# Kernel tuning notes

Measured on AMD Instinct MI355X. Metric: run time of the kernel, lower is better.

Reference implementation:

```python
import jax, jax.numpy as jnp
import numpy as np

DETER, STOCH, ACT, HID, RANK, B = 2048, 1024, 12, 1024, 16, 16384
EPS = 1e-4


def rmsnorm(x, w, eps=EPS):
    # RMSNorm with learnable scale (torch nn.RMSNorm default affine)
    return x * jax.lax.rsqrt(jnp.mean(x * x, axis=-1, keepdims=True) + eps) * w


def setup_inputs() -> dict:
    key = jax.random.key(0)
    ks = jax.random.split(key, 16)
    s = 0.02
    return {
        "stoch": jax.random.normal(ks[0], (B, 32, 32), jnp.float32),
        "deter": jax.random.normal(ks[1], (B, DETER), jnp.float32),
        "action": jax.random.normal(ks[2], (B, ACT), jnp.float32),
        "W1": jax.random.normal(ks[3], (STOCH + ACT, HID), jnp.float32) * s,
        "b1": jnp.zeros((HID,), jnp.float32),
        "g1": jnp.ones((HID,), jnp.float32),
        "W2": jax.random.normal(ks[4], (HID, DETER), jnp.float32) * s,
        "b2": jnp.zeros((DETER,), jnp.float32),
        "Wu": jax.random.normal(ks[5], (DETER, RANK), jnp.float32) * s,
        "Wv": jax.random.normal(ks[6], (RANK, DETER), jnp.float32) * s,
        "a_log": jnp.zeros((DETER,), jnp.float32),
        "dt_p": jnp.zeros((DETER,), jnp.float32),
        "Wg": jax.random.normal(ks[7], (2 * DETER, DETER), jnp.float32) * s,
        "bg": jnp.zeros((DETER,), jnp.float32),
        "Wc": jax.random.normal(ks[8], (2 * DETER, DETER), jnp.float32) * s,
        "bc": jnp.zeros((DETER,), jnp.float32),
        "gn": jnp.ones((DETER,), jnp.float32),
    }


def reference(stoch, deter, action, W1, b1, g1, W2, b2, Wu, Wv, a_log, dt_p,
              Wg, bg, Wc, bc, gn):
    bsz = action.shape[0]
    s = stoch.reshape(bsz, -1)
    # action / clip(|action|, min=1) with detached denominator
    denom = jax.lax.stop_gradient(jnp.maximum(jnp.abs(action), 1.0))
    a_n = action / denom
    # input MLP: Linear -> RMSNorm -> SiLU -> Linear
    x = jnp.concatenate([s, a_n], axis=-1) @ W1 + b1
    x = jax.nn.silu(rmsnorm(x, g1))
    inp = x @ W2 + b2                                # [B, deter]
    # low-rank state mixing
    mixed = deter + (deter @ Wu) @ Wv                # [B, deter]
    dt = jax.nn.softplus(dt_p)[None, :] + 1e-4       # [1, deter]
    a = -jax.nn.softplus(a_log)[None, :]
    ssm = jnp.exp(a * dt) * mixed + dt * inp
    joint = jnp.concatenate([ssm, inp], axis=-1)     # [B, 2*deter]
    gate = jax.nn.sigmoid(joint @ Wg + bg)
    cand = jnp.tanh(joint @ Wc + bc)
    out = gate * cand + (1.0 - gate) * deter
    return rmsnorm(out, gn)
```

## Files before the change

kernel.cpp:

```cpp
#include <hip/hip_runtime.h>
#include <hip/hip_bf16.h>
#include <stdint.h>

#define DETER 2048
#define STOCH 1024
#define ACT   12
#define HID   1024
#define RANK  16
#define BSZ   16384
#define K1P   1056

typedef unsigned short u16;
typedef __attribute__((ext_vector_type(8))) short short8;
typedef __attribute__((ext_vector_type(4))) float f32x4;

__device__ __forceinline__ float bf2f(u16 u) {
  union { uint32_t i; float f; } c; c.i = ((uint32_t)u) << 16; return c.f;
}
__device__ __forceinline__ u16 f2bf(float f) {
  union { float f; uint32_t u; } c; c.f = f;
  uint32_t r = ((c.u >> 16) & 1u) + 0x7fffu;
  return (u16)((c.u + r) >> 16);
}
__device__ __forceinline__ float sigmoidf_(float x) { return 1.f / (1.f + expf(-x)); }
__device__ __forceinline__ float softplusf_(float x) { return (x > 20.f) ? x : log1pf(expf(x)); }

__device__ __forceinline__ void gload_lds16(const void* g, void* l) {
  __builtin_amdgcn_global_load_lds((const __attribute__((address_space(1))) void*)g,
                                   (__attribute__((address_space(3))) void*)l, 16, 0, 0);
}

#define SZ_WBT1 ((size_t)1024 * K1P * 2)
#define SZ_WBT2 ((size_t)DETER * HID * 2)
#define SZ_WBTG ((size_t)DETER * (2 * DETER) * 2)
#define SZ_XIN  ((size_t)BSZ * K1P * 2)
#define SZ_H    ((size_t)BSZ * HID * 2)
#define SZ_XPRE ((size_t)BSZ * HID * 4)
#define SZ_J    ((size_t)BSZ * (2 * DETER) * 2)

#define O_WBT1 ((size_t)0)
#define O_WBT2 (O_WBT1 + SZ_WBT1)
#define O_WBTG (O_WBT2 + SZ_WBT2)
#define O_WBTC (O_WBTG + SZ_WBTG)
#define O_E    (O_WBTC + SZ_WBTG)
#define O_DTV  (O_E + 8192)
#define O_XIN  (O_DTV + 8192)
#define O_H    (O_XIN + SZ_XIN)
#define O_XPRE (O_H + SZ_H)
#define O_J    (O_XPRE + SZ_XPRE)
#define O_CPRE O_XIN
#define O_SSMA O_XPRE
#define O_GPRE O_XPRE
#define WS_NEED (O_J + SZ_J)

__global__ void prep_params(const float* __restrict__ a_log, const float* __restrict__ dt_p,
                            float* __restrict__ ev, float* __restrict__ dtv) {
  int j = blockIdx.x * 256 + threadIdx.x;
  if (j < DETER) {
    float dt = softplusf_(dt_p[j]) + 1e-4f;
    float a  = -softplusf_(a_log[j]);
    ev[j]  = expf(a * dt);
    dtv[j] = dt;
  }
}

__global__ void transpose_w(const float* __restrict__ in, u16* __restrict__ out,
                            int K, int N, int Kp) {
  __shared__ float tile[32][33];
  int k0 = blockIdx.x * 32, n0 = blockIdx.y * 32;
  int tx = threadIdx.x, ty = threadIdx.y;
  #pragma unroll
  for (int r = 0; r < 4; ++r) {
    int k = k0 + ty + r * 8;
    tile[ty + r * 8][tx] = (k < K) ? in[(size_t)k * N + n0 + tx] : 0.f;
  }
  __syncthreads();
  #pragma unroll
  for (int r = 0; r < 4; ++r) {
    int n = n0 + ty + r * 8;
    out[(size_t)n * Kp + k0 + tx] = f2bf(tile[tx][ty + r * 8]);
  }
}

__global__ void build_xin(const float* __restrict__ stoch, const float* __restrict__ action,
                          u16* __restrict__ Xin) {
  int idx = blockIdx.x * 256 + threadIdx.x;
  if (idx >= BSZ * 132) return;
  int b = idx / 132, c = idx % 132;
  union { u16 us[8]; uint4 u; } pk;
  if (c < 128) {
    const float4* p = (const float4*)(stoch + (size_t)b * 1024 + c * 8);
    float4 x = p[0], y = p[1];
    pk.us[0] = f2bf(x.x); pk.us[1] = f2bf(x.y); pk.us[2] = f2bf(x.z); pk.us[3] = f2bf(x.w);
    pk.us[4] = f2bf(y.x); pk.us[5] = f2bf(y.y); pk.us[6] = f2bf(y.z); pk.us[7] = f2bf(y.w);
  } else {
    #pragma unroll
    for (int e = 0; e < 8; ++e) {
      int col = c * 8 + e - 1024;
      float v = 0.f;
      if (col < ACT) {
        float a = action[(size_t)b * ACT + col];
        v = a / fmaxf(fabsf(a), 1.f);
      }
      pk.us[e] = f2bf(v);
    }
  }
  *(uint4*)(Xin + (size_t)b * K1P + c * 8) = pk.u;
}

template <int EPI>
__global__ void gemm_bt(const u16* __restrict__ A, const u16* __restrict__ Bt,
                        int K, int N,
                        const float* __restrict__ bias,
                        const u16* __restrict__ ssmA, const float* __restrict__ dtv,
                        float* __restrict__ outF, u16* __restrict__ outH,
                        u16* __restrict__ J) {
  __shared__ __attribute__((aligned(16))) u16 sA[128 * 32];
  __shared__ __attribute__((aligned(16))) u16 sB[128 * 32];

  int nwg = gridDim.x * gridDim.y;
  int flat = blockIdx.y * gridDim.x + blockIdx.x;
  int q = nwg >> 3;
  int wg = (flat & 7) * q + (flat >> 3);
  int by = wg / gridDim.x, bx = wg % gridDim.x;

  int blockRow = by * 128, blockCol = bx * 128;
  int tid = threadIdx.x;
  int wid = tid >> 6, lane = tid & 63;
  int wr = wid >> 1, wc = wid & 1;
  int l16 = lane & 15, lq = lane >> 4;
  int srow = lane >> 2;
  int scol = (lane & 3) * 8;

  f32x4 acc[4][4];
  #pragma unroll
  for (int i = 0; i < 4; ++i)
    #pragma unroll
    for (int j = 0; j < 4; ++j) acc[i][j] = (f32x4){0.f, 0.f, 0.f, 0.f};

  const u16* aP = A + (size_t)blockRow * K + scol;
  const u16* bP = Bt + (size_t)blockCol * K + scol;
  int c0 = wid * 2, c1 = wid * 2 + 1;

  for (int kk = 0; kk < K; kk += 32) {
    gload_lds16(aP + (size_t)(c0 * 16 + srow) * K + kk, &sA[c0 * 512]);
    gload_lds16(aP + (size_t)(c1 * 16 + srow) * K + kk, &sA[c1 * 512]);
    gload_lds16(bP + (size_t)(c0 * 16 + srow) * K + kk, &sB[c0 * 512]);
    gload_lds16(bP + (size_t)(c1 * 16 + srow) * K + kk, &sB[c1 * 512]);
    __syncthreads();

    short8 af[4], bf[4];
    #pragma unroll
    for (int i = 0; i < 4; ++i)
      af[i] = *(const short8*)&sA[(wr * 64 + i * 16 + l16) * 32 + lq * 8];
    #pragma unroll
    for (int j = 0; j < 4; ++j)
      bf[j] = *(const short8*)&sB[(wc * 64 + j * 16 + l16) * 32 + lq * 8];
    #pragma unroll
    for (int i = 0; i < 4; ++i)
      #pragma unroll
      for (int j = 0; j < 4; ++j)
        acc[i][j] = __builtin_amdgcn_mfma_f32_16x16x32_bf16(af[i], bf[j], acc[i][j], 0, 0, 0);
    __syncthreads();
  }

  #pragma unroll
  for (int i = 0; i < 4; ++i) {
    int row0 = blockRow + wr * 64 + i * 16 + lq * 4;
    #pragma unroll
    for (int j = 0; j < 4; ++j) {
      int col = blockCol + wc * 64 + j * 16 + l16;
      float bv = bias[col];
      float dv = (EPI == 1) ? dtv[col] : 0.f;
      #pragma unroll
      for (int r = 0; r < 4; ++r) {
        size_t row = (size_t)(row0 + r);
        float v = acc[i][j][r] + bv;
        if (EPI == 0) {
          outF[row * N + col] = v;
        } else if (EPI == 2) {
          outH[row * N + col] = f2bf(v);
        } else {
          float ssm = bf2f(ssmA[row * N + col]) + dv * v;
          J[row * (2 * N) + col]     = f2bf(ssm);
          J[row * (2 * N) + N + col] = f2bf(v);
        }
      }
    }
  }
}

__global__ void rmsnorm_silu_k(const float* __restrict__ X, const float* __restrict__ g1,
                               u16* __restrict__ H) {
  int b = blockIdx.x, t = threadIdx.x;
  const float4* x4 = (const float4*)(X + (size_t)b * HID);
  float4 v = x4[t];
  float ss = v.x * v.x + v.y * v.y + v.z * v.z + v.w * v.w;
  #pragma unroll
  for (int m = 32; m >= 1; m >>= 1) ss += __shfl_xor(ss, m, 64);
  __shared__ float red[4];
  if ((t & 63) == 0) red[t >> 6] = ss;
  __syncthreads();
  float tot = red[0] + red[1] + red[2] + red[3];
  float rms = rsqrtf(tot * (1.f / HID) + 1e-4f);
  float4 g = ((const float4*)g1)[t];
  float z0 = v.x * rms * g.x, z1 = v.y * rms * g.y, z2 = v.z * rms * g.z, z3 = v.w * rms * g.w;
  union { u16 us[4]; uint2 u; } pk;
  pk.us[0] = f2bf(z0 * sigmoidf_(z0));
  pk.us[1] = f2bf(z1 * sigmoidf_(z1));
  pk.us[2] = f2bf(z2 * sigmoidf_(z2));
  pk.us[3] = f2bf(z3 * sigmoidf_(z3));
  *(uint2*)(H + (size_t)b * HID + t * 4) = pk.u;
}

__global__ void mix_k(const float* __restrict__ deter, const float* __restrict__ Wu,
                      const float* __restrict__ Wv, const float* __restrict__ ev,
                      u16* __restrict__ ssmA) {
  __shared__ __attribute__((aligned(16))) float ld[4][DETER];
  __shared__ float part[16][16][4];
  __shared__ float ts[4][16];
  int b0 = blockIdx.x * 4, t = threadIdx.x;
  #pragma unroll
  for (int rr = 0; rr < 4; ++rr) {
    const float4* src = (const float4*)(deter + (size_t)(b0 + rr) * DETER);
    ((float4*)ld[rr])[t]       = src[t];
    ((float4*)ld[rr])[t + 256] = src[t + 256];
  }
  __syncthreads();
  int r = t & 15, chunk = t >> 4;
  float accv[4] = {0.f, 0.f, 0.f, 0.f};
  for (int i = 0; i < 128; ++i) {
    int k = i * 16 + chunk;
    float w = Wu[(size_t)k * RANK + r];
    #pragma unroll
    for (int rr = 0; rr < 4; ++rr) accv[rr] += ld[rr][k] * w;
  }
  #pragma unroll
  for (int rr = 0; rr < 4; ++rr) part[chunk][r][rr] = accv[rr];
  __syncthreads();
  if (t < 64) {
    int rr = t >> 4, r2 = t & 15;
    float s = 0.f;
    #pragma unroll
    for (int c2 = 0; c2 < 16; ++c2) s += part[c2][r2][rr];
    ts[rr][r2] = s;
  }
  __syncthreads();
  #pragma unroll
  for (int jj = 0; jj < 8; ++jj) {
    int j = jj * 256 + t;
    float wv[16];
    #pragma unroll
    for (int r2 = 0; r2 < 16; ++r2) wv[r2] = Wv[(size_t)r2 * DETER + j];
    float ej = ev[j];
    #pragma unroll
    for (int rr = 0; rr < 4; ++rr) {
      float m = ld[rr][j];
      #pragma unroll
      for (int r2 = 0; r2 < 16; ++r2) m += ts[rr][r2] * wv[r2];
      ssmA[(size_t)(b0 + rr) * DETER + j] = f2bf(ej * m);
    }
  }
}

__global__ void final_k(const u16* __restrict__ Gpre, const u16* __restrict__ Cpre,
                        const float* __restrict__ deter, const float* __restrict__ gn,
                        float* __restrict__ out) {
  int b = blockIdx.x, t = threadIdx.x;
  size_t base = (size_t)b * DETER;
  union { uint4 u; u16 us[8]; } pg, pc;
  pg.u = ((const uint4*)(Gpre + base))[t];
  pc.u = ((const uint4*)(Cpre + base))[t];
  const float4* d4 = (const float4*)(deter + base);
  float4 d0 = d4[t * 2], d1 = d4[t * 2 + 1];
  float dv[8] = {d0.x, d0.y, d0.z, d0.w, d1.x, d1.y, d1.z, d1.w};
  float o[8];
  float ss = 0.f;
  #pragma unroll
  for (int e = 0; e < 8; ++e) {
    float g = sigmoidf_(bf2f(pg.us[e]));
    float c = tanhf(bf2f(pc.us[e]));
    o[e] = g * c + (1.f - g) * dv[e];
    ss += o[e] * o[e];
  }
  #pragma unroll
  for (int m = 32; m >= 1; m >>= 1) ss += __shfl_xor(ss, m, 64);
  __shared__ float red[4];
  if ((t & 63) == 0) red[t >> 6] = ss;
  __syncthreads();
  float tot = red[0] + red[1] + red[2] + red[3];
  float rms = rsqrtf(tot * (1.f / DETER) + 1e-4f);
  #pragma unroll
  for (int e = 0; e < 8; ++e)
    out[base + t * 8 + e] = o[e] * rms * gn[t * 8 + e];
}

extern "C" void kernel_launch(void* const* d_in, const int* in_sizes, int n_in,
                              void* d_out, int out_size, void* d_ws, size_t ws_size,
                              hipStream_t stream) {
  const float* stoch  = (const float*)d_in[0];
  const float* deter  = (const float*)d_in[1];
  const float* action = (const float*)d_in[2];
  const float* W1 = (const float*)d_in[3];
  const float* b1 = (const float*)d_in[4];
  const float* g1 = (const float*)d_in[5];
  const float* W2 = (const float*)d_in[6];
  const float* b2 = (const float*)d_in[7];
  const float* Wu = (const float*)d_in[8];
  const float* Wv = (const float*)d_in[9];
  const float* a_log = (const float*)d_in[10];
  const float* dt_p  = (const float*)d_in[11];
  const float* Wg = (const float*)d_in[12];
  const float* bg = (const float*)d_in[13];
  const float* Wc = (const float*)d_in[14];
  const float* bc = (const float*)d_in[15];
  const float* gn = (const float*)d_in[16];

  if (ws_size < WS_NEED) return;

  char* ws = (char*)d_ws;
  u16*   Wbt1 = (u16*)(ws + O_WBT1);
  u16*   Wbt2 = (u16*)(ws + O_WBT2);
  u16*   WbtG = (u16*)(ws + O_WBTG);
  u16*   WbtC = (u16*)(ws + O_WBTC);
  float* ev   = (float*)(ws + O_E);
  float* dtv  = (float*)(ws + O_DTV);
  u16*   Xin  = (u16*)(ws + O_XIN);
  u16*   H    = (u16*)(ws + O_H);
  float* Xpre = (float*)(ws + O_XPRE);
  u16*   ssmA = (u16*)(ws + O_SSMA);
  u16*   Gpre = (u16*)(ws + O_GPRE);
  u16*   Cpre = (u16*)(ws + O_CPRE);
  u16*   J    = (u16*)(ws + O_J);
  float* out  = (float*)d_out;

  dim3 tb(256);

  prep_params<<<dim3(8), tb, 0, stream>>>(a_log, dt_p, ev, dtv);
  transpose_w<<<dim3(K1P / 32, 1024 / 32), dim3(32, 8), 0, stream>>>(W1, Wbt1, STOCH + ACT, HID, K1P);
  transpose_w<<<dim3(HID / 32, DETER / 32), dim3(32, 8), 0, stream>>>(W2, Wbt2, HID, DETER, HID);
  transpose_w<<<dim3((2 * DETER) / 32, DETER / 32), dim3(32, 8), 0, stream>>>(Wg, WbtG, 2 * DETER, DETER, 2 * DETER);
  transpose_w<<<dim3((2 * DETER) / 32, DETER / 32), dim3(32, 8), 0, stream>>>(Wc, WbtC, 2 * DETER, DETER, 2 * DETER);
  build_xin<<<dim3(BSZ * 132 / 256), tb, 0, stream>>>(stoch, action, Xin);

  gemm_bt<0><<<dim3(HID / 128, BSZ / 128), tb, 0, stream>>>(
      Xin, Wbt1, K1P, HID, b1, nullptr, nullptr, Xpre, nullptr, nullptr);
  rmsnorm_silu_k<<<dim3(BSZ), tb, 0, stream>>>(Xpre, g1, H);
  mix_k<<<dim3(BSZ / 4), tb, 0, stream>>>(deter, Wu, Wv, ev, ssmA);
  gemm_bt<1><<<dim3(DETER / 128, BSZ / 128), tb, 0, stream>>>(
      H, Wbt2, HID, DETER, b2, ssmA, dtv, nullptr, nullptr, J);
  gemm_bt<2><<<dim3(DETER / 128, BSZ / 128), tb, 0, stream>>>(
      J, WbtG, 2 * DETER, DETER, bg, nullptr, nullptr, nullptr, Gpre, nullptr);
  gemm_bt<2><<<dim3(DETER / 128, BSZ / 128), tb, 0, stream>>>(
      J, WbtC, 2 * DETER, DETER, bc, nullptr, nullptr, nullptr, Cpre, nullptr);
  final_k<<<dim3(BSZ), tb, 0, stream>>>(Gpre, Cpre, deter, gn, out);
}
```

Before: 1.340 ms.

## Use 256x256 multi-buffered GEMM and merge gate/candidate GEMMs

```diff
diff --git a/kernel.cpp b/kernel.cpp
--- a/kernel.cpp
+++ b/kernel.cpp
@@ -29,6 +29,9 @@
   __builtin_amdgcn_global_load_lds((const __attribute__((address_space(1))) void*)g,
                                    (__attribute__((address_space(3))) void*)l, 16, 0, 0);
 }
+__device__ __forceinline__ void wait_lgkm0() { asm volatile("s_waitcnt lgkmcnt(0)" ::: "memory"); }
+template <int N>
+__device__ __forceinline__ void wait_vm() { asm volatile("s_waitcnt vmcnt(%0)" :: "n"(N) : "memory"); }
 
 #define SZ_WBT1 ((size_t)1024 * K1P * 2)
 #define SZ_WBT2 ((size_t)DETER * HID * 2)
@@ -44,23 +47,27 @@
 #define O_WBTC (O_WBTG + SZ_WBTG)
 #define O_E    (O_WBTC + SZ_WBTG)
 #define O_DTV  (O_E + 8192)
-#define O_XIN  (O_DTV + 8192)
+#define O_BGC  (O_DTV + 8192)
+#define O_XIN  (O_BGC + 16384)
 #define O_H    (O_XIN + SZ_XIN)
 #define O_XPRE (O_H + SZ_H)
 #define O_J    (O_XPRE + SZ_XPRE)
-#define O_CPRE O_XIN
 #define O_SSMA O_XPRE
-#define O_GPRE O_XPRE
+#define O_GC   O_XIN
 #define WS_NEED (O_J + SZ_J)
 
 __global__ void prep_params(const float* __restrict__ a_log, const float* __restrict__ dt_p,
-                            float* __restrict__ ev, float* __restrict__ dtv) {
+                            const float* __restrict__ bg, const float* __restrict__ bc,
+                            float* __restrict__ ev, float* __restrict__ dtv,
+                            float* __restrict__ biasGC) {
   int j = blockIdx.x * 256 + threadIdx.x;
   if (j < DETER) {
     float dt = softplusf_(dt_p[j]) + 1e-4f;
     float a  = -softplusf_(a_log[j]);
     ev[j]  = expf(a * dt);
     dtv[j] = dt;
+    biasGC[j]         = bg[j];
+    biasGC[DETER + j] = bc[j];
   }
 }
 
@@ -109,67 +116,109 @@
 }
 
 template <int EPI>
-__global__ void gemm_bt(const u16* __restrict__ A, const u16* __restrict__ Bt,
-                        int K, int N,
+__launch_bounds__(512, 2)
+__global__ void gemm256(const u16* __restrict__ A, const u16* __restrict__ Bt,
+                        int K, int N, int NT,
                         const float* __restrict__ bias,
                         const u16* __restrict__ ssmA, const float* __restrict__ dtv,
                         float* __restrict__ outF, u16* __restrict__ outH,
                         u16* __restrict__ J) {
-  __shared__ __attribute__((aligned(16))) u16 sA[128 * 32];
-  __shared__ __attribute__((aligned(16))) u16 sB[128 * 32];
+  __shared__ __attribute__((aligned(16))) u16 sA[4][256 * 32];
+  __shared__ __attribute__((aligned(16))) u16 sB[4][256 * 32];
 
   int nwg = gridDim.x * gridDim.y;
   int flat = blockIdx.y * gridDim.x + blockIdx.x;
   int q = nwg >> 3;
   int wg = (flat & 7) * q + (flat >> 3);
   int by = wg / gridDim.x, bx = wg % gridDim.x;
-
-  int blockRow = by * 128, blockCol = bx * 128;
+  int blockRow = by * 256, blockCol = bx * 256;
+
   int tid = threadIdx.x;
   int wid = tid >> 6, lane = tid & 63;
-  int wr = wid >> 1, wc = wid & 1;
+  int wm = wid >> 2, wn = wid & 3;
   int l16 = lane & 15, lq = lane >> 4;
-  int srow = lane >> 2;
-  int scol = (lane & 3) * 8;
-
-  f32x4 acc[4][4];
-  #pragma unroll
-  for (int i = 0; i < 4; ++i)
+  int xq = l16 >> 2;
+
+  int p0 = tid, p1 = tid + 512;
+  int r0 = p0 >> 2, g0 = (p0 & 3) ^ ((r0 >> 2) & 3);
+  int r1 = p1 >> 2, g1 = (p1 & 3) ^ ((r1 >> 2) & 3);
+  const u16* a0 = A + (size_t)(blockRow + r0) * K + g0 * 8;
+  const u16* a1 = A + (size_t)(blockRow + r1) * K + g1 * 8;
+  const u16* b0 = Bt + (size_t)(blockCol + r0) * K + g0 * 8;
+  const u16* b1 = Bt + (size_t)(blockCol + r1) * K + g1 * 8;
+  int ldsg0 = (wid * 64) * 8;
+  int ldsg1 = (512 + wid * 64) * 8;
+
+  auto STAGE_A = [&](int t) {
+    int kt = (t < NT ? t : NT - 1) * 32;
+    int buf = t & 3;
+    gload_lds16(a0 + kt, &sA[buf][ldsg0]);
+    gload_lds16(a1 + kt, &sA[buf][ldsg1]);
+  };
+  auto STAGE_B = [&](int t) {
+    int kt = (t < NT ? t : NT - 1) * 32;
+    int buf = t & 3;
+    gload_lds16(b0 + kt, &sB[buf][ldsg0]);
+    gload_lds16(b1 + kt, &sB[buf][ldsg1]);
+  };
+
+  f32x4 acc[8][4];
+  #pragma unroll
+  for (int i = 0; i < 8; ++i)
     #pragma unroll
     for (int j = 0; j < 4; ++j) acc[i][j] = (f32x4){0.f, 0.f, 0.f, 0.f};
 
-  const u16* aP = A + (size_t)blockRow * K + scol;
-  const u16* bP = Bt + (size_t)blockCol * K + scol;
-  int c0 = wid * 2, c1 = wid * 2 + 1;
-
-  for (int kk = 0; kk < K; kk += 32) {
-    gload_lds16(aP + (size_t)(c0 * 16 + srow) * K + kk, &sA[c0 * 512]);
-    gload_lds16(aP + (size_t)(c1 * 16 + srow) * K + kk, &sA[c1 * 512]);
-    gload_lds16(bP + (size_t)(c0 * 16 + srow) * K + kk, &sB[c0 * 512]);
-    gload_lds16(bP + (size_t)(c1 * 16 + srow) * K + kk, &sB[c1 * 512]);
-    __syncthreads();
-
+  int aBase = (wm * 128 + l16) * 32 + ((lq ^ xq) * 8);
+  int bBase = (wn * 64 + l16) * 32 + ((lq ^ xq) * 8);
+
+  STAGE_A(0); STAGE_B(0);
+  STAGE_A(1); STAGE_B(1);
+  STAGE_A(2); STAGE_B(2);
+  wait_vm<8>();
+  __builtin_amdgcn_s_barrier();
+
+  for (int t = 0; t < NT; ++t) {
+    int buf = t & 3;
+    const u16* pA = &sA[buf][aBase];
+    const u16* pB = &sB[buf][bBase];
     short8 af[4], bf[4];
     #pragma unroll
-    for (int i = 0; i < 4; ++i)
-      af[i] = *(const short8*)&sA[(wr * 64 + i * 16 + l16) * 32 + lq * 8];
-    #pragma unroll
-    for (int j = 0; j < 4; ++j)
-      bf[j] = *(const short8*)&sB[(wc * 64 + j * 16 + l16) * 32 + lq * 8];
+    for (int j = 0; j < 4; ++j) bf[j] = *(const short8*)&pB[j * 512];
+    #pragma unroll
+    for (int i = 0; i < 4; ++i) af[i] = *(const short8*)&pA[i * 512];
+    STAGE_A(t + 3);
+    __builtin_amdgcn_s_barrier();
+    wait_lgkm0();
+    __builtin_amdgcn_s_setprio(1);
     #pragma unroll
     for (int i = 0; i < 4; ++i)
       #pragma unroll
       for (int j = 0; j < 4; ++j)
         acc[i][j] = __builtin_amdgcn_mfma_f32_16x16x32_bf16(af[i], bf[j], acc[i][j], 0, 0, 0);
-    __syncthreads();
-  }
-
-  #pragma unroll
-  for (int i = 0; i < 4; ++i) {
-    int row0 = blockRow + wr * 64 + i * 16 + lq * 4;
+    __builtin_amdgcn_s_setprio(0);
+    __builtin_amdgcn_s_barrier();
+    #pragma unroll
+    for (int i = 0; i < 4; ++i) af[i] = *(const short8*)&pA[2048 + i * 512];
+    STAGE_B(t + 3);
+    __builtin_amdgcn_s_barrier();
+    wait_lgkm0();
+    __builtin_amdgcn_s_setprio(1);
+    #pragma unroll
+    for (int i = 0; i < 4; ++i)
+      #pragma unroll
+      for (int j = 0; j < 4; ++j)
+        acc[4 + i][j] = __builtin_amdgcn_mfma_f32_16x16x32_bf16(af[i], bf[j], acc[4 + i][j], 0, 0, 0);
+    __builtin_amdgcn_s_setprio(0);
+    wait_vm<8>();
+    __builtin_amdgcn_s_barrier();
+  }
+
+  #pragma unroll
+  for (int i = 0; i < 8; ++i) {
+    int row0 = blockRow + wm * 128 + i * 16 + lq * 4;
     #pragma unroll
     for (int j = 0; j < 4; ++j) {
-      int col = blockCol + wc * 64 + j * 16 + l16;
+      int col = blockCol + wn * 64 + j * 16 + l16;
       float bv = bias[col];
       float dv = (EPI == 1) ? dtv[col] : 0.f;
       #pragma unroll
@@ -263,14 +312,14 @@
   }
 }
 
-__global__ void final_k(const u16* __restrict__ Gpre, const u16* __restrict__ Cpre,
-                        const float* __restrict__ deter, const float* __restrict__ gn,
-                        float* __restrict__ out) {
+__global__ void final_k(const u16* __restrict__ GC, const float* __restrict__ deter,
+                        const float* __restrict__ gn, float* __restrict__ out) {
   int b = blockIdx.x, t = threadIdx.x;
   size_t base = (size_t)b * DETER;
+  size_t base2 = (size_t)b * (2 * DETER);
   union { uint4 u; u16 us[8]; } pg, pc;
-  pg.u = ((const uint4*)(Gpre + base))[t];
-  pc.u = ((const uint4*)(Cpre + base))[t];
+  pg.u = ((const uint4*)(GC + base2))[t];
+  pc.u = ((const uint4*)(GC + base2 + DETER))[t];
   const float4* d4 = (const float4*)(deter + base);
   float4 d0 = d4[t * 2], d1 = d4[t * 2 + 1];
   float dv[8] = {d0.x, d0.y, d0.z, d0.w, d1.x, d1.y, d1.z, d1.w};
@@ -319,39 +368,37 @@
   if (ws_size < WS_NEED) return;
 
   char* ws = (char*)d_ws;
-  u16*   Wbt1 = (u16*)(ws + O_WBT1);
-  u16*   Wbt2 = (u16*)(ws + O_WBT2);
-  u16*   WbtG = (u16*)(ws + O_WBTG);
-  u16*   WbtC = (u16*)(ws + O_WBTC);
-  float* ev   = (float*)(ws + O_E);
-  float* dtv  = (float*)(ws + O_DTV);
-  u16*   Xin  = (u16*)(ws + O_XIN);
-  u16*   H    = (u16*)(ws + O_H);
-  float* Xpre = (float*)(ws + O_XPRE);
-  u16*   ssmA = (u16*)(ws + O_SSMA);
-  u16*   Gpre = (u16*)(ws + O_GPRE);
-  u16*   Cpre = (u16*)(ws + O_CPRE);
-  u16*   J    = (u16*)(ws + O_J);
-  float* out  = (float*)d_out;
+  u16*   Wbt1  = (u16*)(ws + O_WBT1);
+  u16*   Wbt2  = (u16*)(ws + O_WBT2);
+  u16*   WbtGC = (u16*)(ws + O_WBTG);
+  u16*   WbtC  = (u16*)(ws + O_WBTC);
+  float* ev    = (float*)(ws + O_E);
+  float* dtv   = (float*)(ws + O_DTV);
+  float* biasGC= (float*)(ws + O_BGC);
+  u16*   Xin   = (u16*)(ws + O_XIN);
+  u16*   H     = (u16*)(ws + O_H);
+  float* Xpre  = (float*)(ws + O_XPRE);
+  u16*   ssmA  = (u16*)(ws + O_SSMA);
+  u16*   GC    = (u16*)(ws + O_GC);
+  u16*   J     = (u16*)(ws + O_J);
+  float* out   = (float*)d_out;
 
   dim3 tb(256);
 
-  prep_params<<<dim3(8), tb, 0, stream>>>(a_log, dt_p, ev, dtv);
+  prep_params<<<dim3(8), tb, 0, stream>>>(a_log, dt_p, bg, bc, ev, dtv, biasGC);
   transpose_w<<<dim3(K1P / 32, 1024 / 32), dim3(32, 8), 0, stream>>>(W1, Wbt1, STOCH + ACT, HID, K1P);
   transpose_w<<<dim3(HID / 32, DETER / 32), dim3(32, 8), 0, stream>>>(W2, Wbt2, HID, DETER, HID);
-  transpose_w<<<dim3((2 * DETER) / 32, DETER / 32), dim3(32, 8), 0, stream>>>(Wg, WbtG, 2 * DETER, DETER, 2 * DETER);
+  transpose_w<<<dim3((2 * DETER) / 32, DETER / 32), dim3(32, 8), 0, stream>>>(Wg, WbtGC, 2 * DETER, DETER, 2 * DETER);
   transpose_w<<<dim3((2 * DETER) / 32, DETER / 32), dim3(32, 8), 0, stream>>>(Wc, WbtC, 2 * DETER, DETER, 2 * DETER);
   build_xin<<<dim3(BSZ * 132 / 256), tb, 0, stream>>>(stoch, action, Xin);
 
-  gemm_bt<0><<<dim3(HID / 128, BSZ / 128), tb, 0, stream>>>(
-      Xin, Wbt1, K1P, HID, b1, nullptr, nullptr, Xpre, nullptr, nullptr);
+  gemm256<0><<<dim3(1024 / 256, BSZ / 256), dim3(512), 0, stream>>>(
+      Xin, Wbt1, K1P, HID, K1P / 32, b1, nullptr, nullptr, Xpre, nullptr, nullptr);
   rmsnorm_silu_k<<<dim3(BSZ), tb, 0, stream>>>(Xpre, g1, H);
   mix_k<<<dim3(BSZ / 4), tb, 0, stream>>>(deter, Wu, Wv, ev, ssmA);
-  gemm_bt<1><<<dim3(DETER / 128, BSZ / 128), tb, 0, stream>>>(
-      H, Wbt2, HID, DETER, b2, ssmA, dtv, nullptr, nullptr, J);
-  gemm_bt<2><<<dim3(DETER / 128, BSZ / 128), tb, 0, stream>>>(
-      J, WbtG, 2 * DETER, DETER, bg, nullptr, nullptr, nullptr, Gpre, nullptr);
-  gemm_bt<2><<<dim3(DETER / 128, BSZ / 128), tb, 0, stream>>>(
-      J, WbtC, 2 * DETER, DETER, bc, nullptr, nullptr, nullptr, Cpre, nullptr);
-  final_k<<<dim3(BSZ), tb, 0, stream>>>(Gpre, Cpre, deter, gn, out);
-}
+  gemm256<1><<<dim3(DETER / 256, BSZ / 256), dim3(512), 0, stream>>>(
+      H, Wbt2, HID, DETER, HID / 32, b2, ssmA, dtv, nullptr, nullptr, J);
+  gemm256<2><<<dim3((2 * DETER) / 256, BSZ / 256), dim3(512), 0, stream>>>(
+      J, WbtGC, 2 * DETER, 2 * DETER, (2 * DETER) / 32, biasGC, nullptr, nullptr, nullptr, GC, nullptr);
+  final_k<<<dim3(BSZ), tb, 0, stream>>>(GC, deter, gn, out);
+}
```

After: 1.434 ms. 1.07x slower.
